# Kernel optimization log

Hardware: AMD Instinct MI355X
Metric: run time of the kernel (lower is better)

The kernel has to match this reference:

```python
import jax, jax.numpy as jnp
import numpy as np

N = 2048


def setup_inputs() -> dict:
    key = jax.random.key(0)
    k1, k2 = jax.random.split(key)
    graph1 = jax.random.uniform(k1, (N, N), dtype=jnp.float32)
    graph2 = jax.random.uniform(k2, (N, N), dtype=jnp.float32)
    return {"graph1": graph1, "graph2": graph2}


def _degree_dist(adj):
    return adj.sum(axis=-1)


def _clustering(adj):
    # diag(A @ A @ A) computed without materializing the full cube:
    # tri_i = sum_j (A@A)_{ij} * A_{ji}
    a2 = adj @ adj                      # [n, n]
    tri = (a2 * adj.T).sum(axis=-1)     # [n]
    deg = adj.sum(axis=-1)
    deg = jnp.where(deg < 2, 1.0, deg)  # torch: deg[deg < 2] = 1
    return tri / (deg * (deg - 1.0))


def reference(graph1, graph2):
    d1 = _degree_dist(graph1)
    d2 = _degree_dist(graph2)
    degree_sim = jnp.exp(-jnp.abs(d1 - d2).mean())
    c1 = _clustering(graph1)
    c2 = _clustering(graph2)
    cluster_sim = jnp.exp(-jnp.abs(c1 - c2).mean())
    overall = (degree_sim + cluster_sim) / 2.0
    return (degree_sim, cluster_sim, overall)
```

## Files before the change

kernel.cpp:

```cpp
#include <hip/hip_runtime.h>

#define NN 2048

typedef unsigned short u16;
typedef __attribute__((ext_vector_type(8))) short short8;
typedef __attribute__((ext_vector_type(4))) float floatx4;

__device__ __forceinline__ u16 f2bf(float f) {
  unsigned u = __float_as_uint(f);
  u += 0x7FFF + ((u >> 16) & 1);
  return (u16)(u >> 16);
}

__device__ __forceinline__ float bf2f(u16 h) {
  return __uint_as_float(((unsigned)h) << 16);
}

__device__ __forceinline__ void load_lds16(const u16* g, u16* l) {
  __builtin_amdgcn_global_load_lds(
      (const __attribute__((address_space(1))) unsigned int*)g,
      (__attribute__((address_space(3))) unsigned int*)l,
      16, 0, 0);
}

__global__ __launch_bounds__(256) void prep_kernel(
    const float* __restrict__ A1, const float* __restrict__ A2,
    u16* __restrict__ Abf, u16* __restrict__ AbfT,
    float* __restrict__ degp, float* __restrict__ tri) {
  __shared__ u16 Tl[64][68];
  const int bx = blockIdx.x, by = blockIdx.y, bz = blockIdx.z;
  const float* __restrict__ A = bz ? A2 : A1;
  u16* __restrict__ ab = Abf + (size_t)bz * (NN * (size_t)NN);
  u16* __restrict__ at = AbfT + (size_t)bz * (NN * (size_t)NN);
  float* __restrict__ dp = degp + (size_t)bz * (32 * NN);
  const int t = threadIdx.x;
  const int r0 = by * 64, c0 = bx * 64;
  const int rs = t >> 4, cs = t & 15;

  if (bx == 0 && t < 64) tri[bz * NN + by * 64 + t] = 0.f;

#pragma unroll
  for (int it = 0; it < 4; ++it) {
    const int r = it * 16 + rs;
    const float4 fv = *(const float4*)(A + (size_t)(r0 + r) * NN + c0 + cs * 4);
    ushort4 b;
    b.x = f2bf(fv.x); b.y = f2bf(fv.y); b.z = f2bf(fv.z); b.w = f2bf(fv.w);
    *(ushort4*)(ab + (size_t)(r0 + r) * NN + c0 + cs * 4) = b;
    Tl[r][cs * 4 + 0] = b.x; Tl[r][cs * 4 + 1] = b.y;
    Tl[r][cs * 4 + 2] = b.z; Tl[r][cs * 4 + 3] = b.w;
    float s = fv.x + fv.y + fv.z + fv.w;
    s += __shfl_xor(s, 1); s += __shfl_xor(s, 2);
    s += __shfl_xor(s, 4); s += __shfl_xor(s, 8);
    if (cs == 0) dp[bx * NN + r0 + r] = s;
  }
  __syncthreads();
#pragma unroll
  for (int it = 0; it < 4; ++it) {
    const int c = it * 16 + rs;
    ushort4 b;
    b.x = Tl[cs * 4 + 0][c]; b.y = Tl[cs * 4 + 1][c];
    b.z = Tl[cs * 4 + 2][c]; b.w = Tl[cs * 4 + 3][c];
    *(ushort4*)(at + (size_t)(c0 + c) * NN + r0 + cs * 4) = b;
  }
}

__global__ __launch_bounds__(256) void gemm_tri_kernel(
    const u16* __restrict__ Abf, const u16* __restrict__ AbfT,
    float* __restrict__ tri) {
  __shared__ u16 smem[17408];

  const int tid = threadIdx.x;
  const int w = tid >> 6, lane = tid & 63;
  const int wm = w >> 1, wn = w & 1;
  const int cl = lane & 15, g = lane >> 4;
  const int i0 = blockIdx.y * 128, j0 = blockIdx.x * 128;
  const size_t mat = (size_t)blockIdx.z * (NN * (size_t)NN);
  const u16* __restrict__ Am = Abf + mat;
  const u16* __restrict__ ATm = AbfT + mat;
  float* __restrict__ triM = tri + blockIdx.z * NN;

  const int s0 = (w * 2 + 0) * 64 + lane;
  const int s1 = (w * 2 + 1) * 64 + lane;
  const int r0s = s0 >> 2, c0s = (s0 & 3) ^ ((r0s >> 1) & 3);
  const int r1s = s1 >> 2, c1s = (s1 & 3) ^ ((r1s >> 1) & 3);
  const u16* gA0 = Am + (size_t)(i0 + r0s) * NN + c0s * 8;
  const u16* gA1 = Am + (size_t)(i0 + r1s) * NN + c1s * 8;
  const u16* gB0 = ATm + (size_t)(j0 + r0s) * NN + c0s * 8;
  const u16* gB1 = ATm + (size_t)(j0 + r1s) * NN + c1s * 8;
  u16* lA0 = smem + (w * 2 + 0) * 512;
  u16* lA1 = smem + (w * 2 + 1) * 512;
  u16* lB0 = smem + 4096 + (w * 2 + 0) * 512;
  u16* lB1 = smem + 4096 + (w * 2 + 1) * 512;

  const int swz = g ^ ((cl >> 1) & 3);
  int aoff[4], boff[4];
#pragma unroll
  for (int tm = 0; tm < 4; ++tm)
    aoff[tm] = (wm * 64 + tm * 16 + cl) * 32 + swz * 8;
#pragma unroll
  for (int tn = 0; tn < 4; ++tn)
    boff[tn] = 4096 + (wn * 64 + tn * 16 + cl) * 32 + swz * 8;

  floatx4 acc[4][4] = {};

  for (int k0 = 0; k0 < NN; k0 += 32) {
    __syncthreads();
    load_lds16(gA0 + k0, lA0);
    load_lds16(gA1 + k0, lA1);
    load_lds16(gB0 + k0, lB0);
    load_lds16(gB1 + k0, lB1);
    __syncthreads();

    short8 af[4], bfr[4];
#pragma unroll
    for (int tm = 0; tm < 4; ++tm)
      af[tm] = *(const short8*)(smem + aoff[tm]);
#pragma unroll
    for (int tn = 0; tn < 4; ++tn)
      bfr[tn] = *(const short8*)(smem + boff[tn]);
#pragma unroll
    for (int tm = 0; tm < 4; ++tm)
#pragma unroll
      for (int tn = 0; tn < 4; ++tn)
        acc[tm][tn] = __builtin_amdgcn_mfma_f32_16x16x32_bf16(
            af[tm], bfr[tn], acc[tm][tn], 0, 0, 0);
  }

  __syncthreads();
#pragma unroll
  for (int it = 0; it < 8; ++it) {
    const int idx = tid + it * 256;
    const int r = idx >> 4, co = (idx & 15) * 8;
    *(uint4*)(smem + r * 136 + co) =
        *(const uint4*)(ATm + (size_t)(i0 + r) * NN + j0 + co);
  }
  __syncthreads();

#pragma unroll
  for (int tm = 0; tm < 4; ++tm) {
#pragma unroll
    for (int reg = 0; reg < 4; ++reg) {
      const int rloc = wm * 64 + tm * 16 + g * 4 + reg;
      float v = 0.f;
#pragma unroll
      for (int tn = 0; tn < 4; ++tn) {
        const int cloc = wn * 64 + tn * 16 + cl;
        v += acc[tm][tn][reg] * bf2f(smem[rloc * 136 + cloc]);
      }
      v += __shfl_xor(v, 1);
      v += __shfl_xor(v, 2);
      v += __shfl_xor(v, 4);
      v += __shfl_xor(v, 8);
      if (cl == 0) atomicAdd(&triM[i0 + rloc], v);
    }
  }
}

__global__ __launch_bounds__(1024) void finalize_kernel(
    const float* __restrict__ degp, const float* __restrict__ tri,
    float* __restrict__ out) {
  __shared__ float red[32];
  const int t = threadIdx.x;
  float sdd = 0.f, scc = 0.f;
  for (int r = t; r < NN; r += 1024) {
    float d1 = 0.f, d2 = 0.f;
#pragma unroll
    for (int p = 0; p < 32; ++p) {
      d1 += degp[p * NN + r];
      d2 += degp[32 * NN + p * NN + r];
    }
    const float t1 = tri[r], t2 = tri[NN + r];
    const float e1 = d1 < 2.f ? 1.f : d1;
    const float e2 = d2 < 2.f ? 1.f : d2;
    sdd += fabsf(d1 - d2);
    scc += fabsf(t1 / (e1 * (e1 - 1.f)) - t2 / (e2 * (e2 - 1.f)));
  }
#pragma unroll
  for (int m = 1; m < 64; m <<= 1) {
    sdd += __shfl_xor(sdd, m);
    scc += __shfl_xor(scc, m);
  }
  const int wv = t >> 6, ln = t & 63;
  if (ln == 0) { red[wv] = sdd; red[16 + wv] = scc; }
  __syncthreads();
  if (t == 0) {
    float a = 0.f, b = 0.f;
#pragma unroll
    for (int i = 0; i < 16; ++i) { a += red[i]; b += red[16 + i]; }
    const float ds = expf(-a * (1.f / (float)NN));
    const float cs = expf(-b * (1.f / (float)NN));
    out[0] = ds;
    out[1] = cs;
    out[2] = 0.5f * (ds + cs);
  }
}

extern "C" void kernel_launch(void* const* d_in, const int* in_sizes, int n_in,
                              void* d_out, int out_size, void* d_ws, size_t ws_size,
                              hipStream_t stream) {
  (void)in_sizes; (void)n_in; (void)out_size; (void)ws_size;
  const float* A1 = (const float*)d_in[0];
  const float* A2 = (const float*)d_in[1];
  float* out = (float*)d_out;

  u16* Abf = (u16*)d_ws;
  u16* AbfT = Abf + 2 * (size_t)NN * NN;
  float* tri = (float*)(AbfT + 2 * (size_t)NN * NN);
  float* degp = tri + 2 * NN;

  prep_kernel<<<dim3(32, 32, 2), 256, 0, stream>>>(A1, A2, Abf, AbfT, degp, tri);
  gemm_tri_kernel<<<dim3(16, 16, 2), 256, 0, stream>>>(Abf, AbfT, tri);
  finalize_kernel<<<1, 1024, 0, stream>>>(degp, tri, out);
}
```

Measured before the change: 133.3 us.

## Double-buffer GEMM LDS loads and parallelize degree finalize across blocks

The GEMM main loop now uses two LDS buffers: while the current K-slice is consumed by MFMAs, the next slice is prefetched with global_load_lds, using explicit waitcnt and barriers in place of two __syncthreads per iteration. The degree partial sums are stored row-major so a multi-block finalize can read them with coalesced float4 loads. The single-block finalize is split into a 16-block partial reduction plus a tiny final kernel. This trades an extra kernel launch and hand-written waitcnt encodings for overlapping global-load latency with compute and a faster reduction.

```diff
diff --git a/kernel.cpp b/kernel.cpp
--- a/kernel.cpp
+++ b/kernel.cpp
@@ -51,7 +51,7 @@
     float s = fv.x + fv.y + fv.z + fv.w;
     s += __shfl_xor(s, 1); s += __shfl_xor(s, 2);
     s += __shfl_xor(s, 4); s += __shfl_xor(s, 8);
-    if (cs == 0) dp[bx * NN + r0 + r] = s;
+    if (cs == 0) dp[(r0 + r) * 32 + bx] = s;
   }
   __syncthreads();
 #pragma unroll
@@ -87,10 +87,8 @@
   const u16* gA1 = Am + (size_t)(i0 + r1s) * NN + c1s * 8;
   const u16* gB0 = ATm + (size_t)(j0 + r0s) * NN + c0s * 8;
   const u16* gB1 = ATm + (size_t)(j0 + r1s) * NN + c1s * 8;
-  u16* lA0 = smem + (w * 2 + 0) * 512;
-  u16* lA1 = smem + (w * 2 + 1) * 512;
-  u16* lB0 = smem + 4096 + (w * 2 + 0) * 512;
-  u16* lB1 = smem + 4096 + (w * 2 + 1) * 512;
+  const int sA0 = (w * 2 + 0) * 512, sA1 = (w * 2 + 1) * 512;
+  const int sB0 = 4096 + sA0, sB1 = 4096 + sA1;
 
   const int swz = g ^ ((cl >> 1) & 3);
   int aoff[4], boff[4];
@@ -103,21 +101,42 @@
 
   floatx4 acc[4][4] = {};
 
-  for (int k0 = 0; k0 < NN; k0 += 32) {
-    __syncthreads();
-    load_lds16(gA0 + k0, lA0);
-    load_lds16(gA1 + k0, lA1);
-    load_lds16(gB0 + k0, lB0);
-    load_lds16(gB1 + k0, lB1);
-    __syncthreads();
-
+  {
+    u16* base = smem;
+    load_lds16(gA0, base + sA0);
+    load_lds16(gA1, base + sA1);
+    load_lds16(gB0, base + sB0);
+    load_lds16(gB1, base + sB1);
+  }
+
+  for (int it = 0; it < 64; ++it) {
+    const int p = it & 1;
+    asm volatile("" ::: "memory");
+    __builtin_amdgcn_s_barrier();
+    asm volatile("" ::: "memory");
+    if (it < 63) {
+      const int kk = (it + 1) * 32;
+      u16* base = smem + (p ^ 1) * 8192;
+      load_lds16(gA0 + kk, base + sA0);
+      load_lds16(gA1 + kk, base + sA1);
+      load_lds16(gB0 + kk, base + sB0);
+      load_lds16(gB1 + kk, base + sB1);
+      __builtin_amdgcn_s_waitcnt(0x0F74);
+    } else {
+      __builtin_amdgcn_s_waitcnt(0x0F70);
+    }
+    asm volatile("" ::: "memory");
+    __builtin_amdgcn_s_barrier();
+    asm volatile("" ::: "memory");
+
+    const int pb = p * 8192;
     short8 af[4], bfr[4];
 #pragma unroll
     for (int tm = 0; tm < 4; ++tm)
-      af[tm] = *(const short8*)(smem + aoff[tm]);
+      af[tm] = *(const short8*)(smem + pb + aoff[tm]);
 #pragma unroll
     for (int tn = 0; tn < 4; ++tn)
-      bfr[tn] = *(const short8*)(smem + boff[tn]);
+      bfr[tn] = *(const short8*)(smem + pb + boff[tn]);
 #pragma unroll
     for (int tm = 0; tm < 4; ++tm)
 #pragma unroll
@@ -156,27 +175,32 @@
   }
 }
 
-__global__ __launch_bounds__(1024) void finalize_kernel(
+__global__ __launch_bounds__(1024) void finalize1_kernel(
     const float* __restrict__ degp, const float* __restrict__ tri,
-    float* __restrict__ out) {
+    float* __restrict__ part) {
   __shared__ float red[32];
   const int t = threadIdx.x;
+  const int r = blockIdx.x * 128 + (t >> 3);
+  const int q = (t & 7) * 4;
+  const float4 v1 = *(const float4*)(degp + (size_t)r * 32 + q);
+  const float4 v2 = *(const float4*)(degp + 32 * NN + (size_t)r * 32 + q);
+  float d1 = v1.x + v1.y + v1.z + v1.w;
+  float d2 = v2.x + v2.y + v2.z + v2.w;
+#pragma unroll
+  for (int m = 1; m < 8; m <<= 1) {
+    d1 += __shfl_xor(d1, m);
+    d2 += __shfl_xor(d2, m);
+  }
   float sdd = 0.f, scc = 0.f;
-  for (int r = t; r < NN; r += 1024) {
-    float d1 = 0.f, d2 = 0.f;
-#pragma unroll
-    for (int p = 0; p < 32; ++p) {
-      d1 += degp[p * NN + r];
-      d2 += degp[32 * NN + p * NN + r];
-    }
+  if ((t & 7) == 0) {
     const float t1 = tri[r], t2 = tri[NN + r];
     const float e1 = d1 < 2.f ? 1.f : d1;
     const float e2 = d2 < 2.f ? 1.f : d2;
-    sdd += fabsf(d1 - d2);
-    scc += fabsf(t1 / (e1 * (e1 - 1.f)) - t2 / (e2 * (e2 - 1.f)));
-  }
-#pragma unroll
-  for (int m = 1; m < 64; m <<= 1) {
+    sdd = fabsf(d1 - d2);
+    scc = fabsf(t1 / (e1 * (e1 - 1.f)) - t2 / (e2 * (e2 - 1.f)));
+  }
+#pragma unroll
+  for (int m = 8; m < 64; m <<= 1) {
     sdd += __shfl_xor(sdd, m);
     scc += __shfl_xor(scc, m);
   }
@@ -187,6 +211,17 @@
     float a = 0.f, b = 0.f;
 #pragma unroll
     for (int i = 0; i < 16; ++i) { a += red[i]; b += red[16 + i]; }
+    part[blockIdx.x * 2 + 0] = a;
+    part[blockIdx.x * 2 + 1] = b;
+  }
+}
+
+__global__ void finalize2_kernel(const float* __restrict__ part,
+                                 float* __restrict__ out) {
+  if (threadIdx.x == 0) {
+    float a = 0.f, b = 0.f;
+#pragma unroll
+    for (int i = 0; i < 16; ++i) { a += part[i * 2]; b += part[i * 2 + 1]; }
     const float ds = expf(-a * (1.f / (float)NN));
     const float cs = expf(-b * (1.f / (float)NN));
     out[0] = ds;
@@ -207,8 +242,10 @@
   u16* AbfT = Abf + 2 * (size_t)NN * NN;
   float* tri = (float*)(AbfT + 2 * (size_t)NN * NN);
   float* degp = tri + 2 * NN;
+  float* part = degp + 2 * 32 * NN;
 
   prep_kernel<<<dim3(32, 32, 2), 256, 0, stream>>>(A1, A2, Abf, AbfT, degp, tri);
   gemm_tri_kernel<<<dim3(16, 16, 2), 256, 0, stream>>>(Abf, AbfT, tri);
-  finalize_kernel<<<1, 1024, 0, stream>>>(degp, tri, out);
-}
+  finalize1_kernel<<<16, 1024, 0, stream>>>(degp, tri, part);
+  finalize2_kernel<<<1, 64, 0, stream>>>(part, out);
+}
```

Measured after the change: 128.0 us. 1.04x faster.
